# Kernel tuning notes

Hardware: AMD Instinct MI355X
Metric: run time of the kernel (lower is better)

Reference implementation:

```python
import jax, jax.numpy as jnp
import numpy as np

N = 50000      # nodes
E = 800000     # edges (avg degree 16)
G = 128        # g_feat_dim
LG = 16        # lg_feat_dim
CUTOFF = 10.0


def _xavier(key, shape):
    fan_in, fan_out = shape
    lim = float(np.sqrt(6.0 / (fan_in + fan_out)))
    return jax.random.uniform(key, shape, dtype=jnp.float32, minval=-lim, maxval=lim)


def setup_inputs() -> dict:
    key = jax.random.key(0)
    ks = jax.random.split(key, 24)
    inp = {}
    inp["node_s"] = jax.random.normal(ks[0], (N, G), dtype=jnp.float32)
    inp["node_v"] = jax.random.normal(ks[1], (N, 3, G), dtype=jnp.float32)
    inp["edge_s"] = jax.random.normal(ks[2], (E, LG), dtype=jnp.float32)
    inp["edge_v"] = jax.random.normal(ks[3], (E, 3, LG), dtype=jnp.float32)
    inp["dist"] = jax.random.uniform(ks[4], (E,), dtype=jnp.float32) * CUTOFF
    inp["vctr_norm"] = jax.random.normal(ks[5], (E, 3), dtype=jnp.float32)
    inp["src"] = jax.random.randint(ks[6], (E,), 0, N)
    inp["dst"] = jax.random.randint(ks[7], (E,), 0, N)
    # parameters
    inp["Wns"] = _xavier(ks[8], (G, LG));  inp["bns"] = jnp.zeros((LG,), jnp.float32)
    inp["Wnv"] = _xavier(ks[9], (G, LG))   # no bias
    inp["Wen"] = _xavier(ks[10], (2 * LG, LG)); inp["ben"] = jnp.zeros((LG,), jnp.float32)
    inp["Wtp"] = _xavier(ks[11], (LG, LG)); inp["btp"] = jnp.zeros((LG,), jnp.float32)
    inp["Wg1"] = _xavier(ks[12], (LG, LG)); inp["bg1"] = jnp.zeros((LG,), jnp.float32)
    inp["Wg2"] = _xavier(ks[13], (LG, LG)); inp["bg2"] = jnp.zeros((LG,), jnp.float32)
    inp["Wtv"] = _xavier(ks[14], (LG, 3 * LG)); inp["btv"] = jnp.zeros((3 * LG,), jnp.float32)
    inp["Wonv"] = _xavier(ks[15], (LG, G))  # no bias
    inp["Wo1"] = _xavier(ks[16], (2 * LG, LG)); inp["bo1"] = jnp.zeros((LG,), jnp.float32)
    inp["Wo2"] = _xavier(ks[17], (LG, G)); inp["bo2"] = jnp.zeros((G,), jnp.float32)
    inp["ln_g"] = jnp.ones((G,), jnp.float32); inp["ln_b"] = jnp.zeros((G,), jnp.float32)
    inp["cn_scale"] = jnp.ones((G,), jnp.float32)
    return inp


def reference(node_s, node_v, edge_s, edge_v, dist, vctr_norm, src, dst,
              Wns, bns, Wnv, Wen, ben, Wtp, btp, Wg1, bg1, Wg2, bg2,
              Wtv, btv, Wonv, Wo1, bo1, Wo2, bo2, ln_g, ln_b, cn_scale):
    silu = jax.nn.silu
    # node input projections
    ns = silu(node_s @ Wns + bns)                       # [N, LG]
    nv = jnp.einsum('nvg,gl->nvl', node_v, Wnv)         # [N, 3, LG]
    # edge scalar update
    en = jnp.concatenate([ns[src], ns[dst]], axis=-1) @ Wen + ben   # [E, LG]
    tm = en * (edge_s @ Wtp + btp)                                   # [E, LG]
    gate = jax.nn.sigmoid(silu(tm @ Wg1 + bg1) @ Wg2 + bg2)          # GateMLP
    co = 0.5 * (jnp.cos(dist * (np.pi / CUTOFF)) + 1.0) * (dist < CUTOFF)  # cosine cutoff [E]
    es_upd = gate * co[:, None]                                      # [E, LG]
    # edge vector update
    vc = es_upd @ Wtv + btv                                          # [E, 3*LG]
    tc, ec, rc = jnp.split(vc, 3, axis=-1)
    ev_upd = (edge_v * tc[:, None, :]
              + nv[src] * ec[:, None, :]
              + vctr_norm[:, :, None] * rc[:, None, :]) * co[:, None, None]  # [E, 3, LG]
    # scatter-sum to destination nodes
    n_ev = jax.ops.segment_sum(ev_upd, dst, num_segments=N)          # [N, 3, LG]
    n_es = jax.ops.segment_sum(es_upd, dst, num_segments=N)          # [N, LG]
    # node updates
    n_v_upd = jnp.einsum('nvl,lg->nvg', n_ev, Wonv)                  # [N, 3, G]
    nv_norm = jnp.sqrt(jnp.sum(nv * nv, axis=1) + 1e-12)             # [N, LG]
    n_mess = jnp.concatenate([n_es, nv_norm], axis=-1)               # [N, 2*LG]
    n_s_upd = silu(n_mess @ Wo1 + bo1) @ Wo2 + bo2                   # [N, G]
    # residuals
    node_s_out = node_s + n_s_upd
    node_v_out = node_v + n_v_upd
    edge_s_out = edge_s + es_upd
    edge_v_out = edge_v + ev_upd
    # CoorsNorm over spatial axis (dim 1)
    vnorm = jnp.sqrt(jnp.sum(node_v_out ** 2, axis=1, keepdims=True)).clip(1e-8)
    node_v_out = node_v_out / vnorm * cn_scale
    # LayerNorm over features
    mu = node_s_out.mean(-1, keepdims=True)
    var = node_s_out.var(-1, keepdims=True)
    node_s_out = (node_s_out - mu) / jnp.sqrt(var + 1e-5) * ln_g + ln_b
    return (node_s_out, node_v_out, edge_s_out, edge_v_out)
```

## Files before the change

### kernel.cpp

```cpp
#include <hip/hip_runtime.h>
#include <hip/hip_bf16.h>
#include <math.h>

#define NN 50000
#define EE 800000
#define GG 128
#define LGD 16

typedef unsigned int u32;
typedef __hip_bfloat16 bf16;

__device__ __forceinline__ float bflo(u32 u){ union{u32 x; float f;} c; c.x = u << 16; return c.f; }
__device__ __forceinline__ float bfhi(u32 u){ union{u32 x; float f;} c; c.x = u & 0xffff0000u; return c.f; }
__device__ __forceinline__ u32 f2bf(float f){
    union{float f; u32 u;} c; c.f = f;
    return (c.u + 0x7fffu + ((c.u >> 16) & 1u)) >> 16;
}
__device__ __forceinline__ float siluf(float x){ return x / (1.f + expf(-x)); }
__device__ __forceinline__ float sigmf(float x){ return 1.f / (1.f + expf(-x)); }

template<bool F32>
__device__ __forceinline__ float ld1(const void* p, size_t i){
    if (F32) return reinterpret_cast<const float*>(p)[i];
    return __bfloat162float(reinterpret_cast<const bf16*>(p)[i]);
}
template<bool F32>
__device__ __forceinline__ void st1(void* p, size_t i, float v){
    if (F32) reinterpret_cast<float*>(p)[i] = v;
    else reinterpret_cast<unsigned short*>(p)[i] = (unsigned short)f2bf(v);
}
template<bool F32>
__device__ __forceinline__ void ld8v(const void* p, size_t i, float* o){
    if (F32){
        const float4* q = reinterpret_cast<const float4*>(reinterpret_cast<const float*>(p) + i);
        float4 a = q[0], b = q[1];
        o[0]=a.x;o[1]=a.y;o[2]=a.z;o[3]=a.w;o[4]=b.x;o[5]=b.y;o[6]=b.z;o[7]=b.w;
    } else {
        uint4 q = *reinterpret_cast<const uint4*>(reinterpret_cast<const bf16*>(p) + i);
        o[0]=bflo(q.x);o[1]=bfhi(q.x);o[2]=bflo(q.y);o[3]=bfhi(q.y);
        o[4]=bflo(q.z);o[5]=bfhi(q.z);o[6]=bflo(q.w);o[7]=bfhi(q.w);
    }
}
template<bool F32>
__device__ __forceinline__ void ld2v(const void* p, size_t i, float& a, float& b){
    if (F32){ float2 q = *reinterpret_cast<const float2*>(reinterpret_cast<const float*>(p)+i); a=q.x; b=q.y; }
    else { u32 r = *reinterpret_cast<const u32*>(reinterpret_cast<const bf16*>(p)+i); a=bflo(r); b=bfhi(r); }
}
template<bool F32>
__device__ __forceinline__ void st2v(void* p, size_t i, float a, float b){
    if (F32){ *reinterpret_cast<float2*>(reinterpret_cast<float*>(p)+i) = make_float2(a,b); }
    else { *reinterpret_cast<u32*>(reinterpret_cast<bf16*>(p)+i) = f2bf(a) | (f2bf(b)<<16); }
}

__global__ __launch_bounds__(1024) void k_detect(const u32* __restrict__ q, int* __restrict__ flag){
    __shared__ int s;
    if (threadIdx.x == 0) s = 0;
    __syncthreads();
    int h = 0;
    #pragma unroll
    for (int i = 0; i < 4; i++){
        u32 w = q[threadIdx.x + i*1024];
        if ((w & 0x7F80u) == 0x7F80u) h = 1;
    }
    if (h) atomicOr(&s, 1);
    __syncthreads();
    if (threadIdx.x == 0) flag[0] = s;
}

__global__ __launch_bounds__(256) void k_hist(const int* __restrict__ dst, int* __restrict__ cnt){
    const int e = blockIdx.x * 256 + threadIdx.x;
    atomicAdd(&cnt[dst[e]], 1);
}

__global__ __launch_bounds__(256) void k_scan(int* __restrict__ cur, int* __restrict__ off){
    const int S = 196;
    const int t = threadIdx.x;
    const int b0 = t * S;
    int lsum = 0;
    for (int k = 0; k < S; k++){
        int i = b0 + k;
        if (i < NN) lsum += cur[i];
    }
    __shared__ int ssum[256];
    ssum[t] = lsum;
    __syncthreads();
    #pragma unroll
    for (int d = 1; d < 256; d <<= 1){
        int tv = (t >= d) ? ssum[t - d] : 0;
        __syncthreads();
        ssum[t] += tv;
        __syncthreads();
    }
    int run = ssum[t] - lsum;
    for (int k = 0; k < S; k++){
        int i = b0 + k;
        if (i >= NN) break;
        int c = cur[i];
        off[i] = run;
        cur[i] = run;
        run += c;
    }
    if (t == 255) off[NN] = run;
}

__global__ __launch_bounds__(256) void k_fill(const int* __restrict__ dst, int* __restrict__ cur,
                                              int* __restrict__ eidx){
    const int e = blockIdx.x * 256 + threadIdx.x;
    const int p = atomicAdd(&cur[dst[e]], 1);
    eidx[p] = e;
}

template<bool F32>
__global__ __launch_bounds__(256) void k_node_pre(
    const int* __restrict__ mode,
    const void* __restrict__ node_s, const void* __restrict__ node_v,
    const void* __restrict__ Wns, const void* __restrict__ bns,
    const void* __restrict__ Wnv, const void* __restrict__ Wen,
    float* __restrict__ preS, float* __restrict__ preD,
    float* __restrict__ nv, float* __restrict__ nvn)
{
    if ((mode[0] != 0) != F32) return;
    __shared__ float sWns[GG*LGD];
    __shared__ float sWnv[GG*LGD];
    __shared__ float sWen[32*16];
    __shared__ float sb[LGD];
    __shared__ float sbuf[4][512];
    const int tid = threadIdx.x;
    for (int i = tid; i < GG*LGD; i += 256){
        sWns[i] = ld1<F32>(Wns, i);
        sWnv[i] = ld1<F32>(Wnv, i);
    }
    for (int i = tid; i < 512; i += 256) sWen[i] = ld1<F32>(Wen, i);
    if (tid < LGD) sb[tid] = ld1<F32>(bns, tid);
    __syncthreads();

    const int w = tid >> 6, lane = tid & 63, c = lane & 15;
    const int n = blockIdx.x * 4 + w;
    {
        float tmp[8];
        if (lane < 16){
            ld8v<F32>(node_s, (size_t)n*GG + lane*8, tmp);
            float4* dp = reinterpret_cast<float4*>(&sbuf[w][lane*8]);
            dp[0] = make_float4(tmp[0],tmp[1],tmp[2],tmp[3]);
            dp[1] = make_float4(tmp[4],tmp[5],tmp[6],tmp[7]);
        } else {
            ld8v<F32>(node_v, (size_t)n*384 + (lane-16)*8, tmp);
            float4* dp = reinterpret_cast<float4*>(&sbuf[w][128 + (lane-16)*8]);
            dp[0] = make_float4(tmp[0],tmp[1],tmp[2],tmp[3]);
            dp[1] = make_float4(tmp[4],tmp[5],tmp[6],tmp[7]);
        }
    }
    __syncthreads();

    float acc;
    if (lane < 16){
        acc = sb[c];
        #pragma unroll 16
        for (int k = 0; k < GG; k++) acc += sbuf[w][k] * sWns[k*LGD + c];
    } else {
        const int v = (lane >> 4) - 1;
        const float* vb = &sbuf[w][128 + v*128];
        acc = 0.f;
        #pragma unroll 16
        for (int k = 0; k < GG; k++) acc += vb[k] * sWnv[k*LGD + c];
    }
    float v1 = __shfl(acc, 16 + c, 64);
    float v2 = __shfl(acc, 32 + c, 64);
    float v3 = __shfl(acc, 48 + c, 64);
    if (lane < 16){
        const float sns = siluf(acc);
        nvn[(size_t)n*16 + c] = sqrtf(v1*v1 + v2*v2 + v3*v3 + 1e-12f);
        float pS = 0.f, pD = 0.f;
        #pragma unroll
        for (int i = 0; i < 16; i++){
            float x = __shfl(sns, i, 16);
            pS += x * sWen[i*16 + c];
            pD += x * sWen[(16+i)*16 + c];
        }
        preS[(size_t)n*16 + c] = pS;
        preD[(size_t)n*16 + c] = pD;
    } else {
        nv[(size_t)n*48 + (lane - 16)] = acc;
    }
}

template<bool F32>
__global__ __launch_bounds__(256, 3) void k_edge(
    const int* __restrict__ mode,
    const void* __restrict__ edge_s, const void* __restrict__ edge_v,
    const void* __restrict__ dist, const void* __restrict__ vctr,
    const int* __restrict__ src, const int* __restrict__ dst,
    const void* __restrict__ ben,
    const void* __restrict__ Wtp, const void* __restrict__ btp,
    const void* __restrict__ Wg1, const void* __restrict__ bg1,
    const void* __restrict__ Wg2, const void* __restrict__ bg2,
    const void* __restrict__ Wtv, const void* __restrict__ btv,
    const float* __restrict__ preS, const float* __restrict__ preD,
    const float* __restrict__ nv,
    float* __restrict__ esu_o, float* __restrict__ evu_o,
    void* __restrict__ es_out, void* __restrict__ ev_out)
{
    if ((mode[0] != 0) != F32) return;
    const int t = blockIdx.x * 256 + threadIdx.x;
    const int e = t >> 4;
    const int j = t & 15;

    float wtp[16], wg1[16], wg2[16], wT[16], wE[16], wR[16];
    #pragma unroll
    for (int i = 0; i < 16; i++){
        wtp[i] = ld1<F32>(Wtp, i*16 + j);
        wg1[i] = ld1<F32>(Wg1, i*16 + j);
        wg2[i] = ld1<F32>(Wg2, i*16 + j);
        wT[i]  = ld1<F32>(Wtv, i*48 + j);
        wE[i]  = ld1<F32>(Wtv, i*48 + 16 + j);
        wR[i]  = ld1<F32>(Wtv, i*48 + 32 + j);
    }
    const float bben = ld1<F32>(ben, j);
    const float bbtp = ld1<F32>(btp, j);
    const float bbg1 = ld1<F32>(bg1, j);
    const float bbg2 = ld1<F32>(bg2, j);
    const float bT = ld1<F32>(btv, j);
    const float bE = ld1<F32>(btv, 16 + j);
    const float bR = ld1<F32>(btv, 32 + j);

    const int s = src[e], d = dst[e];
    const float dd = ld1<F32>(dist, e);
    const float co = (dd < 10.f) ? 0.5f * (cosf(dd * 0.3141592653589793f) + 1.f) : 0.f;

    const float enj = preS[(size_t)s*16 + j] + preD[(size_t)d*16 + j] + bben;
    const float esj = ld1<F32>(edge_s, (size_t)e*16 + j);

    float tp = bbtp;
    #pragma unroll
    for (int i = 0; i < 16; i++) tp += __shfl(esj, i, 16) * wtp[i];
    const float tmj = enj * tp;

    float a = bbg1;
    #pragma unroll
    for (int i = 0; i < 16; i++) a += __shfl(tmj, i, 16) * wg1[i];
    const float g1j = siluf(a);

    a = bbg2;
    #pragma unroll
    for (int i = 0; i < 16; i++) a += __shfl(g1j, i, 16) * wg2[i];
    const float esuj = sigmf(a) * co;

    esu_o[(size_t)e*16 + j] = esuj;
    st1<F32>(es_out, (size_t)e*16 + j, esj + esuj);

    float vT = bT, vE = bE, vR = bR;
    #pragma unroll
    for (int i = 0; i < 16; i++){
        float x = __shfl(esuj, i, 16);
        vT += x * wT[i];
        vE += x * wE[i];
        vR += x * wR[i];
    }

    #pragma unroll
    for (int v = 0; v < 3; v++){
        const float evj = ld1<F32>(edge_v, (size_t)e*48 + v*16 + j);
        const float nvj = nv[(size_t)s*48 + v*16 + j];
        const float vn  = ld1<F32>(vctr, (size_t)e*3 + v);
        const float u = (evj*vT + nvj*vE + vn*vR) * co;
        st1<F32>(ev_out, (size_t)e*48 + v*16 + j, evj + u);
        if (evu_o) evu_o[(size_t)e*48 + v*16 + j] = u;
    }
}

template<bool F32>
__global__ __launch_bounds__(256) void k_node_post(
    const int* __restrict__ mode,
    const void* __restrict__ node_s, const void* __restrict__ node_v,
    const float* __restrict__ esu_ws, const float* __restrict__ evu,
    const float* __restrict__ nvn, const float* __restrict__ nv,
    const void* __restrict__ edge_v, const void* __restrict__ dist, const void* __restrict__ vctr,
    const int* __restrict__ src,
    const int* __restrict__ off, const int* __restrict__ eidx,
    const void* __restrict__ Wtv, const void* __restrict__ btv,
    const void* __restrict__ Wonv, const void* __restrict__ Wo1, const void* __restrict__ bo1,
    const void* __restrict__ Wo2, const void* __restrict__ bo2,
    const void* __restrict__ ln_g, const void* __restrict__ ln_b, const void* __restrict__ cn,
    void* __restrict__ s_out, void* __restrict__ v_out)
{
    if ((mode[0] != 0) != F32) return;
    __shared__ float sWonv[16*128], sWo2[16*128], sWo1[32*16];
    __shared__ float sbo1[16], sbo2[128], slg[128], slb[128], scn[128];
    __shared__ float smess[4][32], sev[4][48], sh[4][16];
    const int tid = threadIdx.x;
    for (int i = tid; i < 2048; i += 256){
        sWonv[i] = ld1<F32>(Wonv, i);
        sWo2[i]  = ld1<F32>(Wo2, i);
    }
    for (int i = tid; i < 512; i += 256) sWo1[i] = ld1<F32>(Wo1, i);
    if (tid < 16) sbo1[tid] = ld1<F32>(bo1, tid);
    if (tid < 128){
        sbo2[tid] = ld1<F32>(bo2, tid);
        slg[tid]  = ld1<F32>(ln_g, tid);
        slb[tid]  = ld1<F32>(ln_b, tid);
        scn[tid]  = ld1<F32>(cn, tid);
    }

    const int w = tid >> 6, lane = tid & 63;
    const int n = blockIdx.x * 4 + w;
    const int j = lane & 15;
    const int vv = (lane >> 4) - 1;
    const int c48 = lane - 16;

    const int beg = off[n], end = off[n+1];
    float acc = 0.f;

    if (evu){
        const float* gp; int mul, offl;
        if (lane < 16){ gp = esu_ws; mul = 16; offl = j; }
        else          { gp = evu;    mul = 48; offl = c48; }
        int t = beg;
        for (; t + 3 < end; t += 4){
            const int e0 = eidx[t],   e1 = eidx[t+1];
            const int e2 = eidx[t+2], e3 = eidx[t+3];
            const float a0 = gp[(size_t)e0*mul + offl];
            const float a1 = gp[(size_t)e1*mul + offl];
            const float a2 = gp[(size_t)e2*mul + offl];
            const float a3 = gp[(size_t)e3*mul + offl];
            acc += (a0 + a1) + (a2 + a3);
        }
        for (; t < end; ++t)
            acc += gp[(size_t)eidx[t]*mul + offl];
    } else {
        float wT[16], wE[16], wR[16];
        #pragma unroll
        for (int i = 0; i < 16; i++){
            wT[i] = ld1<F32>(Wtv, i*48 + j);
            wE[i] = ld1<F32>(Wtv, i*48 + 16 + j);
            wR[i] = ld1<F32>(Wtv, i*48 + 32 + j);
        }
        const float bT = ld1<F32>(btv, j);
        const float bE = ld1<F32>(btv, 16 + j);
        const float bR = ld1<F32>(btv, 32 + j);
        for (int t = beg; t < end; t++){
            const int e = eidx[t];
            float eu[16];
            {
                const float4* ep = reinterpret_cast<const float4*>(esu_ws + (size_t)e*16);
                float4 q0 = ep[0], q1 = ep[1], q2 = ep[2], q3 = ep[3];
                eu[0]=q0.x;  eu[1]=q0.y;  eu[2]=q0.z;  eu[3]=q0.w;
                eu[4]=q1.x;  eu[5]=q1.y;  eu[6]=q1.z;  eu[7]=q1.w;
                eu[8]=q2.x;  eu[9]=q2.y;  eu[10]=q2.z; eu[11]=q2.w;
                eu[12]=q3.x; eu[13]=q3.y; eu[14]=q3.z; eu[15]=q3.w;
            }
            if (lane < 16){
                acc += eu[j];
            } else {
                float tc = bT, ec = bE, rc = bR;
                #pragma unroll
                for (int i = 0; i < 16; i++){
                    tc += eu[i] * wT[i];
                    ec += eu[i] * wE[i];
                    rc += eu[i] * wR[i];
                }
                const float dd = ld1<F32>(dist, e);
                const float co = (dd < 10.f) ? 0.5f * (cosf(dd * 0.3141592653589793f) + 1.f) : 0.f;
                const int se = src[e];
                const float ev  = ld1<F32>(edge_v, (size_t)e*48 + c48);
                const float nvq = nv[(size_t)se*48 + c48];
                const float vn  = ld1<F32>(vctr, (size_t)e*3 + vv);
                acc += (ev*tc + nvq*ec + vn*rc) * co;
            }
        }
    }

    if (lane < 16){
        smess[w][lane]      = acc;
        smess[w][16 + lane] = nvn[(size_t)n*16 + lane];
    } else {
        sev[w][c48] = acc;
    }
    __syncthreads();

    if (lane < 16){
        float a = sbo1[lane];
        #pragma unroll
        for (int i = 0; i < 32; i++) a += smess[w][i] * sWo1[i*16 + lane];
        sh[w][lane] = siluf(a);
    }
    __syncthreads();

    const int g0 = lane * 2;
    float s0, s1;
    {
        float r0, r1;
        ld2v<F32>(node_s, (size_t)n*128 + g0, r0, r1);
        float a0 = sbo2[g0], a1 = sbo2[g0+1];
        #pragma unroll
        for (int i = 0; i < 16; i++){
            float h = sh[w][i];
            a0 += h * sWo2[i*128 + g0];
            a1 += h * sWo2[i*128 + g0 + 1];
        }
        s0 = r0 + a0;
        s1 = r1 + a1;
    }
    float ssum = s0 + s1, ssq = s0*s0 + s1*s1;
    #pragma unroll
    for (int offd = 32; offd >= 1; offd >>= 1){
        ssum += __shfl_xor(ssum, offd, 64);
        ssq  += __shfl_xor(ssq,  offd, 64);
    }
    const float mean = ssum * (1.f/128.f);
    const float var  = ssq * (1.f/128.f) - mean*mean;
    const float rstd = rsqrtf(var + 1e-5f);
    {
        float o0 = (s0 - mean) * rstd * slg[g0]   + slb[g0];
        float o1 = (s1 - mean) * rstd * slg[g0+1] + slb[g0+1];
        st2v<F32>(s_out, (size_t)n*128 + g0, o0, o1);
    }
    float va[3], vb[3];
    #pragma unroll
    for (int v = 0; v < 3; v++){
        float r0, r1;
        ld2v<F32>(node_v, (size_t)n*384 + v*128 + g0, r0, r1);
        float a0 = 0.f, a1 = 0.f;
        #pragma unroll
        for (int i = 0; i < 16; i++){
            float x = sev[w][v*16 + i];
            a0 += x * sWonv[i*128 + g0];
            a1 += x * sWonv[i*128 + g0 + 1];
        }
        va[v] = r0 + a0;
        vb[v] = r1 + a1;
    }
    float n0 = fmaxf(sqrtf(va[0]*va[0] + va[1]*va[1] + va[2]*va[2]), 1e-8f);
    float n1 = fmaxf(sqrtf(vb[0]*vb[0] + vb[1]*vb[1] + vb[2]*vb[2]), 1e-8f);
    const float sc0 = scn[g0]   / n0;
    const float sc1 = scn[g0+1] / n1;
    #pragma unroll
    for (int v = 0; v < 3; v++){
        st2v<F32>(v_out, (size_t)n*384 + v*128 + g0, va[v]*sc0, vb[v]*sc1);
    }
}

extern "C" void kernel_launch(void* const* d_in, const int* in_sizes, int n_in,
                              void* d_out, int out_size, void* d_ws, size_t ws_size,
                              hipStream_t stream)
{
    (void)in_sizes; (void)n_in; (void)out_size;
    const void* node_s = d_in[0];
    const void* node_v = d_in[1];
    const void* edge_s = d_in[2];
    const void* edge_v = d_in[3];
    const void* dist   = d_in[4];
    const void* vctr   = d_in[5];
    const int*  src    = (const int*)d_in[6];
    const int*  dst    = (const int*)d_in[7];
    const void* Wns = d_in[8];  const void* bns = d_in[9];
    const void* Wnv = d_in[10];
    const void* Wen = d_in[11]; const void* ben = d_in[12];
    const void* Wtp = d_in[13]; const void* btp = d_in[14];
    const void* Wg1 = d_in[15]; const void* bg1 = d_in[16];
    const void* Wg2 = d_in[17]; const void* bg2 = d_in[18];
    const void* Wtv = d_in[19]; const void* btv = d_in[20];
    const void* Wonv= d_in[21];
    const void* Wo1 = d_in[22]; const void* bo1 = d_in[23];
    const void* Wo2 = d_in[24]; const void* bo2 = d_in[25];
    const void* lng = d_in[26]; const void* lnb = d_in[27];
    const void* cn  = d_in[28];

    float* ws    = (float*)d_ws;
    float* preS_ = ws;
    float* preD_ = preS_ + (size_t)NN*16;
    float* nv_   = preD_ + (size_t)NN*16;
    float* nvn_  = nv_   + (size_t)NN*48;
    float* esu_  = nvn_  + (size_t)NN*16;
    int*   off_  = (int*)(esu_ + (size_t)EE*16);
    int*   cur_  = off_ + (NN + 1);
    int*   eidx_ = cur_ + NN;
    int*   flag  = eidx_ + EE;

    size_t used    = (size_t)((char*)(flag + 1) - (char*)d_ws);
    size_t aligned = (used + 255) & ~(size_t)255;
    float* evu_    = (float*)((char*)d_ws + aligned);
    const bool big = ws_size >= aligned + (size_t)EE*48*sizeof(float);
    float* evu_arg = big ? evu_ : nullptr;

    char* ob = (char*)d_out;
    const size_t esz_f32 = 4, esz_b16 = 2;
    const size_t off_v  = (size_t)NN*GG;
    const size_t off_es = off_v + (size_t)NN*3*GG;
    const size_t off_ev = off_es + (size_t)EE*LGD;

    hipMemsetAsync(cur_, 0, (size_t)NN*sizeof(int), stream);
    k_detect<<<1, 1024, 0, stream>>>((const u32*)node_s, flag);

    k_hist<<<EE/256, 256, 0, stream>>>(dst, cur_);
    k_scan<<<1, 256, 0, stream>>>(cur_, off_);
    k_fill<<<EE/256, 256, 0, stream>>>(dst, cur_, eidx_);

    void* s_out_b  = ob;
    void* v_out_b  = ob + off_v  * esz_b16;
    void* es_out_b = ob + off_es * esz_b16;
    void* ev_out_b = ob + off_ev * esz_b16;
    void* s_out_f  = ob;
    void* v_out_f  = ob + off_v  * esz_f32;
    void* es_out_f = ob + off_es * esz_f32;
    void* ev_out_f = ob + off_ev * esz_f32;

    k_node_pre<false><<<NN/4, 256, 0, stream>>>(flag, node_s, node_v, Wns, bns, Wnv, Wen,
        preS_, preD_, nv_, nvn_);
    k_node_pre<true ><<<NN/4, 256, 0, stream>>>(flag, node_s, node_v, Wns, bns, Wnv, Wen,
        preS_, preD_, nv_, nvn_);

    k_edge<false><<<EE/16, 256, 0, stream>>>(flag, edge_s, edge_v, dist, vctr, src, dst,
        ben, Wtp, btp, Wg1, bg1, Wg2, bg2, Wtv, btv,
        preS_, preD_, nv_, esu_, evu_arg, es_out_b, ev_out_b);
    k_edge<true ><<<EE/16, 256, 0, stream>>>(flag, edge_s, edge_v, dist, vctr, src, dst,
        ben, Wtp, btp, Wg1, bg1, Wg2, bg2, Wtv, btv,
        preS_, preD_, nv_, esu_, evu_arg, es_out_f, ev_out_f);

    k_node_post<false><<<NN/4, 256, 0, stream>>>(flag, node_s, node_v, esu_, evu_arg, nvn_, nv_,
        edge_v, dist, vctr, src, off_, eidx_, Wtv, btv,
        Wonv, Wo1, bo1, Wo2, bo2, lng, lnb, cn, s_out_b, v_out_b);
    k_node_post<true ><<<NN/4, 256, 0, stream>>>(flag, node_s, node_v, esu_, evu_arg, nvn_, nv_,
        edge_v, dist, vctr, src, off_, eidx_, Wtv, btv,
        Wonv, Wo1, bo1, Wo2, bo2, lng, lnb, cn, s_out_f, v_out_f);
}
```

Baseline: 1.263 ms.

## Use grid-stride persistent kernels and an interleaved per-edge update buffer

The node-pre, edge and node-post kernels become grid-stride loops over a fixed grid. Weight and bias loads into registers and shared memory are now paid once per block instead of once per small tile. The separate scalar and vector edge-update buffers are merged into one [E,64] record, so the destination-side gather reads 64 contiguous floats per edge across a whole wavefront. Several block barriers inside the loops are dropped on the assumption that each wavefront only touches its own shared slots, which relies on intra-wavefront LDS ordering. The change also removes the occupancy hint on the edge kernel.

```diff
diff --git a/kernel.cpp b/kernel.cpp
--- a/kernel.cpp
+++ b/kernel.cpp
@@ -135,57 +135,59 @@
     __syncthreads();
 
     const int w = tid >> 6, lane = tid & 63, c = lane & 15;
-    const int n = blockIdx.x * 4 + w;
-    {
-        float tmp[8];
+
+    for (int g = blockIdx.x; g < NN/4; g += gridDim.x){
+        const int n = g * 4 + w;
+        {
+            float tmp[8];
+            if (lane < 16){
+                ld8v<F32>(node_s, (size_t)n*GG + lane*8, tmp);
+                float4* dp = reinterpret_cast<float4*>(&sbuf[w][lane*8]);
+                dp[0] = make_float4(tmp[0],tmp[1],tmp[2],tmp[3]);
+                dp[1] = make_float4(tmp[4],tmp[5],tmp[6],tmp[7]);
+            } else {
+                ld8v<F32>(node_v, (size_t)n*384 + (lane-16)*8, tmp);
+                float4* dp = reinterpret_cast<float4*>(&sbuf[w][128 + (lane-16)*8]);
+                dp[0] = make_float4(tmp[0],tmp[1],tmp[2],tmp[3]);
+                dp[1] = make_float4(tmp[4],tmp[5],tmp[6],tmp[7]);
+            }
+        }
+
+        float acc;
         if (lane < 16){
-            ld8v<F32>(node_s, (size_t)n*GG + lane*8, tmp);
-            float4* dp = reinterpret_cast<float4*>(&sbuf[w][lane*8]);
-            dp[0] = make_float4(tmp[0],tmp[1],tmp[2],tmp[3]);
-            dp[1] = make_float4(tmp[4],tmp[5],tmp[6],tmp[7]);
+            acc = sb[c];
+            #pragma unroll 16
+            for (int k = 0; k < GG; k++) acc += sbuf[w][k] * sWns[k*LGD + c];
         } else {
-            ld8v<F32>(node_v, (size_t)n*384 + (lane-16)*8, tmp);
-            float4* dp = reinterpret_cast<float4*>(&sbuf[w][128 + (lane-16)*8]);
-            dp[0] = make_float4(tmp[0],tmp[1],tmp[2],tmp[3]);
-            dp[1] = make_float4(tmp[4],tmp[5],tmp[6],tmp[7]);
-        }
-    }
-    __syncthreads();
-
-    float acc;
-    if (lane < 16){
-        acc = sb[c];
-        #pragma unroll 16
-        for (int k = 0; k < GG; k++) acc += sbuf[w][k] * sWns[k*LGD + c];
-    } else {
-        const int v = (lane >> 4) - 1;
-        const float* vb = &sbuf[w][128 + v*128];
-        acc = 0.f;
-        #pragma unroll 16
-        for (int k = 0; k < GG; k++) acc += vb[k] * sWnv[k*LGD + c];
-    }
-    float v1 = __shfl(acc, 16 + c, 64);
-    float v2 = __shfl(acc, 32 + c, 64);
-    float v3 = __shfl(acc, 48 + c, 64);
-    if (lane < 16){
-        const float sns = siluf(acc);
-        nvn[(size_t)n*16 + c] = sqrtf(v1*v1 + v2*v2 + v3*v3 + 1e-12f);
-        float pS = 0.f, pD = 0.f;
-        #pragma unroll
-        for (int i = 0; i < 16; i++){
-            float x = __shfl(sns, i, 16);
-            pS += x * sWen[i*16 + c];
-            pD += x * sWen[(16+i)*16 + c];
-        }
-        preS[(size_t)n*16 + c] = pS;
-        preD[(size_t)n*16 + c] = pD;
-    } else {
-        nv[(size_t)n*48 + (lane - 16)] = acc;
-    }
-}
-
-template<bool F32>
-__global__ __launch_bounds__(256, 3) void k_edge(
+            const int v = (lane >> 4) - 1;
+            const float* vb = &sbuf[w][128 + v*128];
+            acc = 0.f;
+            #pragma unroll 16
+            for (int k = 0; k < GG; k++) acc += vb[k] * sWnv[k*LGD + c];
+        }
+        float v1 = __shfl(acc, 16 + c, 64);
+        float v2 = __shfl(acc, 32 + c, 64);
+        float v3 = __shfl(acc, 48 + c, 64);
+        if (lane < 16){
+            const float sns = siluf(acc);
+            nvn[(size_t)n*16 + c] = sqrtf(v1*v1 + v2*v2 + v3*v3 + 1e-12f);
+            float pS = 0.f, pD = 0.f;
+            #pragma unroll
+            for (int i = 0; i < 16; i++){
+                float x = __shfl(sns, i, 16);
+                pS += x * sWen[i*16 + c];
+                pD += x * sWen[(16+i)*16 + c];
+            }
+            preS[(size_t)n*16 + c] = pS;
+            preD[(size_t)n*16 + c] = pD;
+        } else {
+            nv[(size_t)n*48 + (lane - 16)] = acc;
+        }
+    }
+}
+
+template<bool F32>
+__global__ __launch_bounds__(256) void k_edge(
     const int* __restrict__ mode,
     const void* __restrict__ edge_s, const void* __restrict__ edge_v,
     const void* __restrict__ dist, const void* __restrict__ vctr,
@@ -197,13 +199,11 @@
     const void* __restrict__ Wtv, const void* __restrict__ btv,
     const float* __restrict__ preS, const float* __restrict__ preD,
     const float* __restrict__ nv,
-    float* __restrict__ esu_o, float* __restrict__ evu_o,
+    float* __restrict__ upd, const int fast,
     void* __restrict__ es_out, void* __restrict__ ev_out)
 {
     if ((mode[0] != 0) != F32) return;
-    const int t = blockIdx.x * 256 + threadIdx.x;
-    const int e = t >> 4;
-    const int j = t & 15;
+    const int j = threadIdx.x & 15;
 
     float wtp[16], wg1[16], wg2[16], wT[16], wE[16], wR[16];
     #pragma unroll
@@ -223,48 +223,54 @@
     const float bE = ld1<F32>(btv, 16 + j);
     const float bR = ld1<F32>(btv, 32 + j);
 
-    const int s = src[e], d = dst[e];
-    const float dd = ld1<F32>(dist, e);
-    const float co = (dd < 10.f) ? 0.5f * (cosf(dd * 0.3141592653589793f) + 1.f) : 0.f;
-
-    const float enj = preS[(size_t)s*16 + j] + preD[(size_t)d*16 + j] + bben;
-    const float esj = ld1<F32>(edge_s, (size_t)e*16 + j);
-
-    float tp = bbtp;
-    #pragma unroll
-    for (int i = 0; i < 16; i++) tp += __shfl(esj, i, 16) * wtp[i];
-    const float tmj = enj * tp;
-
-    float a = bbg1;
-    #pragma unroll
-    for (int i = 0; i < 16; i++) a += __shfl(tmj, i, 16) * wg1[i];
-    const float g1j = siluf(a);
-
-    a = bbg2;
-    #pragma unroll
-    for (int i = 0; i < 16; i++) a += __shfl(g1j, i, 16) * wg2[i];
-    const float esuj = sigmf(a) * co;
-
-    esu_o[(size_t)e*16 + j] = esuj;
-    st1<F32>(es_out, (size_t)e*16 + j, esj + esuj);
-
-    float vT = bT, vE = bE, vR = bR;
-    #pragma unroll
-    for (int i = 0; i < 16; i++){
-        float x = __shfl(esuj, i, 16);
-        vT += x * wT[i];
-        vE += x * wE[i];
-        vR += x * wR[i];
-    }
-
-    #pragma unroll
-    for (int v = 0; v < 3; v++){
-        const float evj = ld1<F32>(edge_v, (size_t)e*48 + v*16 + j);
-        const float nvj = nv[(size_t)s*48 + v*16 + j];
-        const float vn  = ld1<F32>(vctr, (size_t)e*3 + v);
-        const float u = (evj*vT + nvj*vE + vn*vR) * co;
-        st1<F32>(ev_out, (size_t)e*48 + v*16 + j, evj + u);
-        if (evu_o) evu_o[(size_t)e*48 + v*16 + j] = u;
+    const int stride = gridDim.x * 256;
+    for (int t = blockIdx.x * 256 + threadIdx.x; t < EE*16; t += stride){
+        const int e = t >> 4;
+
+        const int s = src[e], d = dst[e];
+        const float dd = ld1<F32>(dist, e);
+        const float co = (dd < 10.f) ? 0.5f * (cosf(dd * 0.3141592653589793f) + 1.f) : 0.f;
+
+        const float enj = preS[(size_t)s*16 + j] + preD[(size_t)d*16 + j] + bben;
+        const float esj = ld1<F32>(edge_s, (size_t)e*16 + j);
+
+        float tp = bbtp;
+        #pragma unroll
+        for (int i = 0; i < 16; i++) tp += __shfl(esj, i, 16) * wtp[i];
+        const float tmj = enj * tp;
+
+        float a = bbg1;
+        #pragma unroll
+        for (int i = 0; i < 16; i++) a += __shfl(tmj, i, 16) * wg1[i];
+        const float g1j = siluf(a);
+
+        a = bbg2;
+        #pragma unroll
+        for (int i = 0; i < 16; i++) a += __shfl(g1j, i, 16) * wg2[i];
+        const float esuj = sigmf(a) * co;
+
+        if (fast) upd[(size_t)e*64 + j] = esuj;
+        else      upd[(size_t)e*16 + j] = esuj;
+        st1<F32>(es_out, (size_t)e*16 + j, esj + esuj);
+
+        float vT = bT, vE = bE, vR = bR;
+        #pragma unroll
+        for (int i = 0; i < 16; i++){
+            float x = __shfl(esuj, i, 16);
+            vT += x * wT[i];
+            vE += x * wE[i];
+            vR += x * wR[i];
+        }
+
+        #pragma unroll
+        for (int v = 0; v < 3; v++){
+            const float evj = ld1<F32>(edge_v, (size_t)e*48 + v*16 + j);
+            const float nvj = nv[(size_t)s*48 + v*16 + j];
+            const float vn  = ld1<F32>(vctr, (size_t)e*3 + v);
+            const float u = (evj*vT + nvj*vE + vn*vR) * co;
+            st1<F32>(ev_out, (size_t)e*48 + v*16 + j, evj + u);
+            if (fast) upd[(size_t)e*64 + 16 + v*16 + j] = u;
+        }
     }
 }
 
@@ -272,7 +278,7 @@
 __global__ __launch_bounds__(256) void k_node_post(
     const int* __restrict__ mode,
     const void* __restrict__ node_s, const void* __restrict__ node_v,
-    const float* __restrict__ esu_ws, const float* __restrict__ evu,
+    const float* __restrict__ upd, const int fast,
     const float* __restrict__ nvn, const float* __restrict__ nv,
     const void* __restrict__ edge_v, const void* __restrict__ dist, const void* __restrict__ vctr,
     const int* __restrict__ src,
@@ -300,142 +306,144 @@
         slb[tid]  = ld1<F32>(ln_b, tid);
         scn[tid]  = ld1<F32>(cn, tid);
     }
+    __syncthreads();
 
     const int w = tid >> 6, lane = tid & 63;
-    const int n = blockIdx.x * 4 + w;
     const int j = lane & 15;
     const int vv = (lane >> 4) - 1;
     const int c48 = lane - 16;
 
-    const int beg = off[n], end = off[n+1];
-    float acc = 0.f;
-
-    if (evu){
-        const float* gp; int mul, offl;
-        if (lane < 16){ gp = esu_ws; mul = 16; offl = j; }
-        else          { gp = evu;    mul = 48; offl = c48; }
-        int t = beg;
-        for (; t + 3 < end; t += 4){
-            const int e0 = eidx[t],   e1 = eidx[t+1];
-            const int e2 = eidx[t+2], e3 = eidx[t+3];
-            const float a0 = gp[(size_t)e0*mul + offl];
-            const float a1 = gp[(size_t)e1*mul + offl];
-            const float a2 = gp[(size_t)e2*mul + offl];
-            const float a3 = gp[(size_t)e3*mul + offl];
-            acc += (a0 + a1) + (a2 + a3);
-        }
-        for (; t < end; ++t)
-            acc += gp[(size_t)eidx[t]*mul + offl];
-    } else {
-        float wT[16], wE[16], wR[16];
+    float wT[16], wE[16], wR[16];
+    float bT = 0.f, bE = 0.f, bR = 0.f;
+    if (!fast){
         #pragma unroll
         for (int i = 0; i < 16; i++){
             wT[i] = ld1<F32>(Wtv, i*48 + j);
             wE[i] = ld1<F32>(Wtv, i*48 + 16 + j);
             wR[i] = ld1<F32>(Wtv, i*48 + 32 + j);
         }
-        const float bT = ld1<F32>(btv, j);
-        const float bE = ld1<F32>(btv, 16 + j);
-        const float bR = ld1<F32>(btv, 32 + j);
-        for (int t = beg; t < end; t++){
-            const int e = eidx[t];
-            float eu[16];
-            {
-                const float4* ep = reinterpret_cast<const float4*>(esu_ws + (size_t)e*16);
-                float4 q0 = ep[0], q1 = ep[1], q2 = ep[2], q3 = ep[3];
-                eu[0]=q0.x;  eu[1]=q0.y;  eu[2]=q0.z;  eu[3]=q0.w;
-                eu[4]=q1.x;  eu[5]=q1.y;  eu[6]=q1.z;  eu[7]=q1.w;
-                eu[8]=q2.x;  eu[9]=q2.y;  eu[10]=q2.z; eu[11]=q2.w;
-                eu[12]=q3.x; eu[13]=q3.y; eu[14]=q3.z; eu[15]=q3.w;
+        bT = ld1<F32>(btv, j);
+        bE = ld1<F32>(btv, 16 + j);
+        bR = ld1<F32>(btv, 32 + j);
+    }
+
+    for (int g = blockIdx.x; g < NN/4; g += gridDim.x){
+        const int n = g * 4 + w;
+        const int beg = off[n], end = off[n+1];
+        float acc = 0.f;
+
+        if (fast){
+            int t = beg;
+            for (; t + 3 < end; t += 4){
+                const int e0 = eidx[t],   e1 = eidx[t+1];
+                const int e2 = eidx[t+2], e3 = eidx[t+3];
+                const float a0 = upd[(size_t)e0*64 + lane];
+                const float a1 = upd[(size_t)e1*64 + lane];
+                const float a2 = upd[(size_t)e2*64 + lane];
+                const float a3 = upd[(size_t)e3*64 + lane];
+                acc += (a0 + a1) + (a2 + a3);
             }
-            if (lane < 16){
-                acc += eu[j];
-            } else {
-                float tc = bT, ec = bE, rc = bR;
-                #pragma unroll
-                for (int i = 0; i < 16; i++){
-                    tc += eu[i] * wT[i];
-                    ec += eu[i] * wE[i];
-                    rc += eu[i] * wR[i];
+            for (; t < end; ++t)
+                acc += upd[(size_t)eidx[t]*64 + lane];
+        } else {
+            for (int t = beg; t < end; t++){
+                const int e = eidx[t];
+                float eu[16];
+                {
+                    const float4* ep = reinterpret_cast<const float4*>(upd + (size_t)e*16);
+                    float4 q0 = ep[0], q1 = ep[1], q2 = ep[2], q3 = ep[3];
+                    eu[0]=q0.x;  eu[1]=q0.y;  eu[2]=q0.z;  eu[3]=q0.w;
+                    eu[4]=q1.x;  eu[5]=q1.y;  eu[6]=q1.z;  eu[7]=q1.w;
+                    eu[8]=q2.x;  eu[9]=q2.y;  eu[10]=q2.z; eu[11]=q2.w;
+                    eu[12]=q3.x; eu[13]=q3.y; eu[14]=q3.z; eu[15]=q3.w;
                 }
-                const float dd = ld1<F32>(dist, e);
-                const float co = (dd < 10.f) ? 0.5f * (cosf(dd * 0.3141592653589793f) + 1.f) : 0.f;
-                const int se = src[e];
-                const float ev  = ld1<F32>(edge_v, (size_t)e*48 + c48);
-                const float nvq = nv[(size_t)se*48 + c48];
-                const float vn  = ld1<F32>(vctr, (size_t)e*3 + vv);
-                acc += (ev*tc + nvq*ec + vn*rc) * co;
+                if (lane < 16){
+                    acc += eu[j];
+                } else {
+                    float tc = bT, ec = bE, rc = bR;
+                    #pragma unroll
+                    for (int i = 0; i < 16; i++){
+                        tc += eu[i] * wT[i];
+                        ec += eu[i] * wE[i];
+                        rc += eu[i] * wR[i];
+                    }
+                    const float dd = ld1<F32>(dist, e);
+                    const float co = (dd < 10.f) ? 0.5f * (cosf(dd * 0.3141592653589793f) + 1.f) : 0.f;
+                    const int se = src[e];
+                    const float ev  = ld1<F32>(edge_v, (size_t)e*48 + c48);
+                    const float nvq = nv[(size_t)se*48 + c48];
+                    const float vn  = ld1<F32>(vctr, (size_t)e*3 + vv);
+                    acc += (ev*tc + nvq*ec + vn*rc) * co;
+                }
             }
         }
-    }
-
-    if (lane < 16){
-        smess[w][lane]      = acc;
-        smess[w][16 + lane] = nvn[(size_t)n*16 + lane];
-    } else {
-        sev[w][c48] = acc;
-    }
-    __syncthreads();
-
-    if (lane < 16){
-        float a = sbo1[lane];
-        #pragma unroll
-        for (int i = 0; i < 32; i++) a += smess[w][i] * sWo1[i*16 + lane];
-        sh[w][lane] = siluf(a);
-    }
-    __syncthreads();
-
-    const int g0 = lane * 2;
-    float s0, s1;
-    {
-        float r0, r1;
-        ld2v<F32>(node_s, (size_t)n*128 + g0, r0, r1);
-        float a0 = sbo2[g0], a1 = sbo2[g0+1];
-        #pragma unroll
-        for (int i = 0; i < 16; i++){
-            float h = sh[w][i];
-            a0 += h * sWo2[i*128 + g0];
-            a1 += h * sWo2[i*128 + g0 + 1];
-        }
-        s0 = r0 + a0;
-        s1 = r1 + a1;
-    }
-    float ssum = s0 + s1, ssq = s0*s0 + s1*s1;
-    #pragma unroll
-    for (int offd = 32; offd >= 1; offd >>= 1){
-        ssum += __shfl_xor(ssum, offd, 64);
-        ssq  += __shfl_xor(ssq,  offd, 64);
-    }
-    const float mean = ssum * (1.f/128.f);
-    const float var  = ssq * (1.f/128.f) - mean*mean;
-    const float rstd = rsqrtf(var + 1e-5f);
-    {
-        float o0 = (s0 - mean) * rstd * slg[g0]   + slb[g0];
-        float o1 = (s1 - mean) * rstd * slg[g0+1] + slb[g0+1];
-        st2v<F32>(s_out, (size_t)n*128 + g0, o0, o1);
-    }
-    float va[3], vb[3];
-    #pragma unroll
-    for (int v = 0; v < 3; v++){
-        float r0, r1;
-        ld2v<F32>(node_v, (size_t)n*384 + v*128 + g0, r0, r1);
-        float a0 = 0.f, a1 = 0.f;
-        #pragma unroll
-        for (int i = 0; i < 16; i++){
-            float x = sev[w][v*16 + i];
-            a0 += x * sWonv[i*128 + g0];
-            a1 += x * sWonv[i*128 + g0 + 1];
-        }
-        va[v] = r0 + a0;
-        vb[v] = r1 + a1;
-    }
-    float n0 = fmaxf(sqrtf(va[0]*va[0] + va[1]*va[1] + va[2]*va[2]), 1e-8f);
-    float n1 = fmaxf(sqrtf(vb[0]*vb[0] + vb[1]*vb[1] + vb[2]*vb[2]), 1e-8f);
-    const float sc0 = scn[g0]   / n0;
-    const float sc1 = scn[g0+1] / n1;
-    #pragma unroll
-    for (int v = 0; v < 3; v++){
-        st2v<F32>(v_out, (size_t)n*384 + v*128 + g0, va[v]*sc0, vb[v]*sc1);
+
+        if (lane < 16){
+            smess[w][lane]      = acc;
+            smess[w][16 + lane] = nvn[(size_t)n*16 + lane];
+        } else {
+            sev[w][c48] = acc;
+        }
+
+        if (lane < 16){
+            float a = sbo1[lane];
+            #pragma unroll
+            for (int i = 0; i < 32; i++) a += smess[w][i] * sWo1[i*16 + lane];
+            sh[w][lane] = siluf(a);
+        }
+
+        const int g0 = lane * 2;
+        float s0, s1;
+        {
+            float r0, r1;
+            ld2v<F32>(node_s, (size_t)n*128 + g0, r0, r1);
+            float a0 = sbo2[g0], a1 = sbo2[g0+1];
+            #pragma unroll
+            for (int i = 0; i < 16; i++){
+                float h = sh[w][i];
+                a0 += h * sWo2[i*128 + g0];
+                a1 += h * sWo2[i*128 + g0 + 1];
+            }
+            s0 = r0 + a0;
+            s1 = r1 + a1;
+        }
+        float ssum = s0 + s1, ssq = s0*s0 + s1*s1;
+        #pragma unroll
+        for (int offd = 32; offd >= 1; offd >>= 1){
+            ssum += __shfl_xor(ssum, offd, 64);
+            ssq  += __shfl_xor(ssq,  offd, 64);
+        }
+        const float mean = ssum * (1.f/128.f);
+        const float var  = ssq * (1.f/128.f) - mean*mean;
+        const float rstd = rsqrtf(var + 1e-5f);
+        {
+            float o0 = (s0 - mean) * rstd * slg[g0]   + slb[g0];
+            float o1 = (s1 - mean) * rstd * slg[g0+1] + slb[g0+1];
+            st2v<F32>(s_out, (size_t)n*128 + g0, o0, o1);
+        }
+        float va[3], vb[3];
+        #pragma unroll
+        for (int v = 0; v < 3; v++){
+            float r0, r1;
+            ld2v<F32>(node_v, (size_t)n*384 + v*128 + g0, r0, r1);
+            float a0 = 0.f, a1 = 0.f;
+            #pragma unroll
+            for (int i = 0; i < 16; i++){
+                float x = sev[w][v*16 + i];
+                a0 += x * sWonv[i*128 + g0];
+                a1 += x * sWonv[i*128 + g0 + 1];
+            }
+            va[v] = r0 + a0;
+            vb[v] = r1 + a1;
+        }
+        float n0 = fmaxf(sqrtf(va[0]*va[0] + va[1]*va[1] + va[2]*va[2]), 1e-8f);
+        float n1 = fmaxf(sqrtf(vb[0]*vb[0] + vb[1]*vb[1] + vb[2]*vb[2]), 1e-8f);
+        const float sc0 = scn[g0]   / n0;
+        const float sc1 = scn[g0+1] / n1;
+        #pragma unroll
+        for (int v = 0; v < 3; v++){
+            st2v<F32>(v_out, (size_t)n*384 + v*128 + g0, va[v]*sc0, vb[v]*sc1);
+        }
     }
 }
 
@@ -470,17 +478,15 @@
     float* preD_ = preS_ + (size_t)NN*16;
     float* nv_   = preD_ + (size_t)NN*16;
     float* nvn_  = nv_   + (size_t)NN*48;
-    float* esu_  = nvn_  + (size_t)NN*16;
-    int*   off_  = (int*)(esu_ + (size_t)EE*16);
+    int*   off_  = (int*)(nvn_ + (size_t)NN*16);
     int*   cur_  = off_ + (NN + 1);
     int*   eidx_ = cur_ + NN;
     int*   flag  = eidx_ + EE;
 
     size_t used    = (size_t)((char*)(flag + 1) - (char*)d_ws);
     size_t aligned = (used + 255) & ~(size_t)255;
-    float* evu_    = (float*)((char*)d_ws + aligned);
-    const bool big = ws_size >= aligned + (size_t)EE*48*sizeof(float);
-    float* evu_arg = big ? evu_ : nullptr;
+    float* upd_    = (float*)((char*)d_ws + aligned);
+    const int fast = (ws_size >= aligned + (size_t)EE*64*sizeof(float)) ? 1 : 0;
 
     char* ob = (char*)d_out;
     const size_t esz_f32 = 4, esz_b16 = 2;
@@ -504,22 +510,22 @@
     void* es_out_f = ob + off_es * esz_f32;
     void* ev_out_f = ob + off_ev * esz_f32;
 
-    k_node_pre<false><<<NN/4, 256, 0, stream>>>(flag, node_s, node_v, Wns, bns, Wnv, Wen,
+    k_node_pre<false><<<1024, 256, 0, stream>>>(flag, node_s, node_v, Wns, bns, Wnv, Wen,
         preS_, preD_, nv_, nvn_);
-    k_node_pre<true ><<<NN/4, 256, 0, stream>>>(flag, node_s, node_v, Wns, bns, Wnv, Wen,
+    k_node_pre<true ><<<1024, 256, 0, stream>>>(flag, node_s, node_v, Wns, bns, Wnv, Wen,
         preS_, preD_, nv_, nvn_);
 
-    k_edge<false><<<EE/16, 256, 0, stream>>>(flag, edge_s, edge_v, dist, vctr, src, dst,
+    k_edge<false><<<2048, 256, 0, stream>>>(flag, edge_s, edge_v, dist, vctr, src, dst,
         ben, Wtp, btp, Wg1, bg1, Wg2, bg2, Wtv, btv,
-        preS_, preD_, nv_, esu_, evu_arg, es_out_b, ev_out_b);
-    k_edge<true ><<<EE/16, 256, 0, stream>>>(flag, edge_s, edge_v, dist, vctr, src, dst,
+        preS_, preD_, nv_, upd_, fast, es_out_b, ev_out_b);
+    k_edge<true ><<<2048, 256, 0, stream>>>(flag, edge_s, edge_v, dist, vctr, src, dst,
         ben, Wtp, btp, Wg1, bg1, Wg2, bg2, Wtv, btv,
-        preS_, preD_, nv_, esu_, evu_arg, es_out_f, ev_out_f);
-
-    k_node_post<false><<<NN/4, 256, 0, stream>>>(flag, node_s, node_v, esu_, evu_arg, nvn_, nv_,
+        preS_, preD_, nv_, upd_, fast, es_out_f, ev_out_f);
+
+    k_node_post<false><<<1024, 256, 0, stream>>>(flag, node_s, node_v, upd_, fast, nvn_, nv_,
         edge_v, dist, vctr, src, off_, eidx_, Wtv, btv,
         Wonv, Wo1, bo1, Wo2, bo2, lng, lnb, cn, s_out_b, v_out_b);
-    k_node_post<true ><<<NN/4, 256, 0, stream>>>(flag, node_s, node_v, esu_, evu_arg, nvn_, nv_,
+    k_node_post<true ><<<1024, 256, 0, stream>>>(flag, node_s, node_v, upd_, fast, nvn_, nv_,
         edge_v, dist, vctr, src, off_, eidx_, Wtv, btv,
         Wonv, Wo1, bo1, Wo2, bo2, lng, lnb, cn, s_out_f, v_out_f);
 }
```

Result: slower. 1.296 ms (+2.6%).
